# Kernel tuning notes

Hardware: AMD Instinct MI355X
Metric: run time of the kernel (lower is better)

Reference implementation:

```python
import jax, jax.numpy as jnp
import numpy as np
import math

B, T, C = 4, 2048, 1024
N_HEAD = 16


def setup_inputs() -> dict:
    key = jax.random.key(0)
    ks = jax.random.split(key, 5)
    s = 0.02
    return {
        "x": jax.random.normal(ks[0], (B, T, C), jnp.float32),
        "W_attn": jax.random.normal(ks[1], (C, 3 * C), jnp.float32) * s,
        "b_attn": jax.random.normal(ks[2], (3 * C,), jnp.float32) * s,
        "W_proj": jax.random.normal(ks[3], (C, C), jnp.float32) * s,
        "b_proj": jax.random.normal(ks[4], (C,), jnp.float32) * s,
    }


def reference(x, W_attn, b_attn, W_proj, b_proj):
    b, t, c = x.shape
    hd = c // N_HEAD  # head dim
    qkv = x @ W_attn + b_attn                       # [B,T,3C]
    q, k, v = jnp.split(qkv, 3, axis=-1)
    # [B,T,C] -> [B,H,T,hd]
    q = q.reshape(b, t, N_HEAD, hd).transpose(0, 2, 1, 3)
    k = k.reshape(b, t, N_HEAD, hd).transpose(0, 2, 1, 3)
    v = v.reshape(b, t, N_HEAD, hd).transpose(0, 2, 1, 3)
    att = jnp.einsum("bhqd,bhkd->bhqk", q, k) * (1.0 / math.sqrt(hd))
    causal = jnp.tril(jnp.ones((t, t), dtype=bool))
    att = jnp.where(causal, att, -jnp.inf)
    att = jax.nn.softmax(att, axis=-1)              # dropout disabled (eval mode)
    y = jnp.einsum("bhqk,bhkd->bhqd", att, v)       # [B,H,T,hd]
    y = y.transpose(0, 2, 1, 3).reshape(b, t, c)
    out = y @ W_proj + b_proj                       # resid dropout disabled (eval)
    return out
```

## Files before the change

### kernel.cpp

```cpp
#include <hip/hip_runtime.h>

#define B_  4
#define T_  2048
#define C_  1024
#define H_  16
#define D_  64
#define BT_ 8192

typedef __bf16 bf16x8 __attribute__((ext_vector_type(8)));
typedef float  f32x4  __attribute__((ext_vector_type(4)));

#define MFMA(a, b, c) __builtin_amdgcn_mfma_f32_16x16x32_bf16((a), (b), (c), 0, 0, 0)
#define LOG2E 1.4426950408889634f

__device__ __forceinline__ float fexp2(float x) {
#if __has_builtin(__builtin_amdgcn_exp2f)
    return __builtin_amdgcn_exp2f(x);
#else
    return __expf(x * 0.6931471805599453f);
#endif
}

__device__ __forceinline__ unsigned short f2bf(float f) {
    union { float f; unsigned u; } v; v.f = f;
    unsigned r = v.u + 0x7FFFu + ((v.u >> 16) & 1u);
    return (unsigned short)(r >> 16);
}

__device__ __forceinline__ void gll16(const unsigned short* g, unsigned short* l) {
    __builtin_amdgcn_global_load_lds((const __attribute__((address_space(1))) void*)g,
                                     (__attribute__((address_space(3))) void*)l, 16, 0, 0);
}

template <int GPR>
__device__ __forceinline__ void stage16(const unsigned short* grow0, size_t stride_us,
                                        unsigned short* lds, int chunk) {
    const int lane = threadIdx.x & 63;
    const int gidx = chunk * 64 + lane;
    const int row  = gidx / GPR, c = gidx % GPR;
    const int csrc = c ^ (row & (GPR - 1));
    gll16(grow0 + (size_t)row * stride_us + csrc * 8, lds + gidx * 8);
}

__global__ __launch_bounds__(256) void prep_kernel(const float* __restrict__ x,
                                                   unsigned short* __restrict__ xb,
                                                   const float* __restrict__ Wa,
                                                   unsigned short* __restrict__ Wab,
                                                   const float* __restrict__ Wp,
                                                   unsigned short* __restrict__ Wpb) {
    __shared__ float tile[32][33];
    const int bid = blockIdx.x;
    if (bid < 8192) {
        int i = bid * 1024 + threadIdx.x * 4;
        float4 v = *(const float4*)&x[i];
        ushort4 o;
        o.x = f2bf(v.x); o.y = f2bf(v.y); o.z = f2bf(v.z); o.w = f2bf(v.w);
        *(ushort4*)&xb[i] = o;
        return;
    }
    const float* in; unsigned short* out; int N, t;
    if (bid < 11264) { t = bid - 8192;  in = Wa; out = Wab; N = 3072; }
    else             { t = bid - 11264; in = Wp; out = Wpb; N = 1024; }
    const int n0 = (t % (N / 32)) * 32, k0 = (t / (N / 32)) * 32;
    const int tr = threadIdx.x >> 3, tc = (threadIdx.x & 7) * 4;
    float4 v = *(const float4*)&in[(size_t)(k0 + tr) * N + n0 + tc];
    tile[tr][tc + 0] = v.x; tile[tr][tc + 1] = v.y;
    tile[tr][tc + 2] = v.z; tile[tr][tc + 3] = v.w;
    __syncthreads();
    ushort4 o;
    o.x = f2bf(tile[tc + 0][tr]);
    o.y = f2bf(tile[tc + 1][tr]);
    o.z = f2bf(tile[tc + 2][tr]);
    o.w = f2bf(tile[tc + 3][tr]);
    *(ushort4*)&out[(size_t)(n0 + tr) * 1024 + k0 + tc] = o;
}

__global__ __launch_bounds__(256) void transpose_v_kernel(const unsigned short* __restrict__ qkv,
                                                          unsigned short* __restrict__ vT) {
    __shared__ unsigned short tile[64][65];
    const int bh = blockIdx.y;
    const int b = bh >> 4, h = bh & 15;
    const int t0 = blockIdx.x * 64;
    const size_t src = (size_t)b * 2048 * 3072 + 2048 + h * 64;
    const size_t dbase = (size_t)bh * (T_ * D_);
    const int r = threadIdx.x >> 2, c = (threadIdx.x & 3) * 16;
    uint4 a0 = *(const uint4*)&qkv[src + (size_t)(t0 + r) * 3072 + c];
    uint4 a1 = *(const uint4*)&qkv[src + (size_t)(t0 + r) * 3072 + c + 8];
    const unsigned short* ap = (const unsigned short*)&a0;
    #pragma unroll
    for (int i = 0; i < 8; ++i) tile[r][c + i] = ap[i];
    ap = (const unsigned short*)&a1;
    #pragma unroll
    for (int i = 0; i < 8; ++i) tile[r][c + 8 + i] = ap[i];
    __syncthreads();
    unsigned short tmp[16];
    #pragma unroll
    for (int i = 0; i < 16; ++i) tmp[i] = tile[c + i][r];
    *(uint4*)&vT[dbase + (size_t)r * T_ + t0 + c]     = *(uint4*)&tmp[0];
    *(uint4*)&vT[dbase + (size_t)r * T_ + t0 + c + 8] = *(uint4*)&tmp[8];
}

template <int MODE, int VDIRECT>
__global__ __launch_bounds__(256) void gemm_bf16_kernel(
    const unsigned short* __restrict__ A,
    const unsigned short* __restrict__ Bt,
    const float* __restrict__ bias,
    float* __restrict__ outF,
    unsigned short* __restrict__ outB,
    unsigned short* __restrict__ vTout,
    int M, int N, int K)
{
    __shared__ __align__(16) unsigned short smem[(MODE == 0 && VDIRECT) ? 10240 : 8192];
    unsigned short* As = smem;
    unsigned short* Bs = smem + 4096;
    const int tid = threadIdx.x;
    const int wave = tid >> 6, lane = tid & 63;
    const int wr = wave >> 1, wc = wave & 1;
    const int g = lane >> 4, li = lane & 15;
    const int m0 = blockIdx.y * 128, n0 = blockIdx.x * 128;

    f32x4 acc[4][4] = {};

    for (int k0 = 0; k0 < K; k0 += 32) {
        __syncthreads();
        stage16<4>(A  + (size_t)m0 * K + k0, K, As, wave * 2);
        stage16<4>(A  + (size_t)m0 * K + k0, K, As, wave * 2 + 1);
        stage16<4>(Bt + (size_t)n0 * K + k0, K, Bs, wave * 2);
        stage16<4>(Bt + (size_t)n0 * K + k0, K, Bs, wave * 2 + 1);
        __syncthreads();
        bf16x8 af[4], bfr[4];
        #pragma unroll
        for (int mi = 0; mi < 4; ++mi) {
            const int row = wr * 64 + mi * 16 + li;
            af[mi] = *(const bf16x8*)&As[row * 32 + ((g ^ (row & 3)) * 8)];
        }
        #pragma unroll
        for (int ni = 0; ni < 4; ++ni) {
            const int row = wc * 64 + ni * 16 + li;
            bfr[ni] = *(const bf16x8*)&Bs[row * 32 + ((g ^ (row & 3)) * 8)];
        }
        #pragma unroll
        for (int mi = 0; mi < 4; ++mi)
            #pragma unroll
            for (int ni = 0; ni < 4; ++ni)
                acc[mi][ni] = MFMA(af[mi], bfr[ni], acc[mi][ni]);
    }

    float bb[4];
    #pragma unroll
    for (int ni = 0; ni < 4; ++ni) bb[ni] = bias[n0 + wc * 64 + ni * 16 + li];

    if (MODE == 0) {
        __syncthreads();
        if (VDIRECT && n0 >= 2048) {
            const int h = (n0 - 2048 + wc * 64) >> 6;
            const int b = m0 >> 11;
            const int tb = (m0 & 2047) + wr * 64;
            unsigned short* vstg = smem + wave * 2560;
            #pragma unroll
            for (int mp = 0; mp < 2; ++mp) {
                #pragma unroll
                for (int mh = 0; mh < 2; ++mh) {
                    const int mi = mp * 2 + mh;
                    #pragma unroll
                    for (int ni = 0; ni < 4; ++ni)
                        #pragma unroll
                        for (int r = 0; r < 4; ++r)
                            vstg[(ni * 16 + li) * 40 + mh * 16 + g * 4 + r]
                                = f2bf(acc[mi][ni][r] + bb[ni]);
                }
                __builtin_amdgcn_wave_barrier();
                uint4 w0 = *(const uint4*)&vstg[lane * 40];
                uint4 w1 = *(const uint4*)&vstg[lane * 40 + 8];
                uint4 w2 = *(const uint4*)&vstg[lane * 40 + 16];
                uint4 w3 = *(const uint4*)&vstg[lane * 40 + 24];
                unsigned short* dp = vTout
                    + (((size_t)(b * 16 + h) * 64 + lane) * 2048 + tb + mp * 32);
                *(uint4*)dp = w0; *(uint4*)&dp[8] = w1;
                *(uint4*)&dp[16] = w2; *(uint4*)&dp[24] = w3;
                __builtin_amdgcn_wave_barrier();
            }
        } else {
            unsigned short* stg = smem + wave * 1152;
            const float qsc = (n0 < 1024) ? 0.125f * LOG2E : 1.0f;
            const int srow = lane & 15, scp = lane >> 4;
            #pragma unroll
            for (int mi = 0; mi < 4; ++mi) {
                #pragma unroll
                for (int ni = 0; ni < 4; ++ni)
                    #pragma unroll
                    for (int r = 0; r < 4; ++r)
                        stg[(g * 4 + r) * 72 + ni * 16 + li] = f2bf((acc[mi][ni][r] + bb[ni]) * qsc);
                __builtin_amdgcn_wave_barrier();
                uint4 w0 = *(const uint4*)&stg[srow * 72 + scp * 16];
                uint4 w1 = *(const uint4*)&stg[srow * 72 + scp * 16 + 8];
                unsigned short* dst = &outB[(size_t)(m0 + wr * 64 + mi * 16 + srow) * N
                                            + n0 + wc * 64 + scp * 16];
                *(uint4*)dst = w0;
                *(uint4*)&dst[8] = w1;
                __builtin_amdgcn_wave_barrier();
            }
        }
    } else {
        #pragma unroll
        for (int mi = 0; mi < 4; ++mi)
            #pragma unroll
            for (int ni = 0; ni < 4; ++ni) {
                const int col = n0 + wc * 64 + ni * 16 + li;
                #pragma unroll
                for (int r = 0; r < 4; ++r)
                    outF[(size_t)(m0 + wr * 64 + mi * 16 + g * 4 + r) * N + col]
                        = acc[mi][ni][r] + bb[ni];
            }
    }
}

__global__ __launch_bounds__(256, 4) void flash_attn_kernel(
    const unsigned short* __restrict__ qkv,
    const unsigned short* __restrict__ vT,
    unsigned short* __restrict__ y)
{
    __shared__ __align__(16) unsigned short Ks[2][64 * 64];
    __shared__ __align__(16) unsigned short Vt[2][64 * 64];
    __shared__ __align__(16) unsigned short Pq[4][16][40];
    const int tid = threadIdx.x;
    const int wv = tid >> 6, lane = tid & 63;
    const int g = lane >> 4, li = lane & 15;
    const int bid = blockIdx.x;
    const int xcd = bid & 7, i = bid >> 3;
    const int bh = xcd * 8 + (i & 7);
    const int p  = i >> 3;
    const int qtA = p, qtB = 31 - p;
    const int b = bh >> 4, h = bh & 15;
    const size_t qrowbase = (size_t)b * 2048 * 3072 + h * 64;
    const size_t vbase = (size_t)bh * (D_ * T_);
    const unsigned short* kbase = qkv + qrowbase + 1024;

    const int rowA = qtA * 64 + wv * 16 + li;
    const int rowB = qtB * 64 + wv * 16 + li;

    bf16x8 aqA[2], aqB[2];
    #pragma unroll
    for (int kc = 0; kc < 2; ++kc) {
        aqA[kc] = *(const bf16x8*)&qkv[qrowbase + (size_t)rowA * 3072 + kc * 32 + g * 8];
        aqB[kc] = *(const bf16x8*)&qkv[qrowbase + (size_t)rowB * 3072 + kc * 32 + g * 8];
    }

    f32x4 oA[4] = {}, oB[4] = {};
    float lA = 0.f, lB = 0.f;
    const float OFS = 8.0f * LOG2E;
    const int nkb = qtB + 1;

    stage16<8>(kbase, 3072, Ks[0], wv * 2);
    stage16<8>(kbase, 3072, Ks[0], wv * 2 + 1);
    stage16<8>(vT + vbase, T_, Vt[0], wv * 2);
    stage16<8>(vT + vbase, T_, Vt[0], wv * 2 + 1);

    for (int kb = 0; kb < nkb; ++kb) {
        const int cur = kb & 1;
        __syncthreads();
        if (kb + 1 < nkb) {
            const int kn = (kb + 1) << 6;
            const int nxt = cur ^ 1;
            stage16<8>(kbase + (size_t)kn * 3072, 3072, Ks[nxt], wv * 2);
            stage16<8>(kbase + (size_t)kn * 3072, 3072, Ks[nxt], wv * 2 + 1);
            stage16<8>(vT + vbase + kn, T_, Vt[nxt], wv * 2);
            stage16<8>(vT + vbase + kn, T_, Vt[nxt], wv * 2 + 1);
        }
        const int k0 = kb << 6;
        const bool doA = (kb <= qtA);
        const unsigned short* ksb = Ks[cur];
        const unsigned short* vtb = Vt[cur];

        #pragma unroll
        for (int half = 0; half < 2; ++half) {
            f32x4 sA[2], sB[2];
            #pragma unroll
            for (int t2 = 0; t2 < 2; ++t2) {
                const int krow = (half * 2 + t2) * 16 + li;
                bf16x8 ka0 = *(const bf16x8*)&ksb[krow * 64 + ((g       ^ (krow & 7)) * 8)];
                bf16x8 ka1 = *(const bf16x8*)&ksb[krow * 64 + (((4 + g) ^ (krow & 7)) * 8)];
                f32x4 z = {};
                z = MFMA(ka0, aqB[0], z);
                sB[t2] = MFMA(ka1, aqB[1], z);
                if (doA) {
                    f32x4 z2 = {};
                    z2 = MFMA(ka0, aqA[0], z2);
                    sA[t2] = MFMA(ka1, aqA[1], z2);
                }
            }
            bf16x8 bpA, bpB;
            {
                #pragma unroll
                for (int t2 = 0; t2 < 2; ++t2) {
                    const int kkb = k0 + (half * 2 + t2) * 16;
                    const bool diag = (kb == qtB);
                    ushort4 pw;
                    #pragma unroll
                    for (int r = 0; r < 4; ++r) {
                        float sv = sB[t2][r];
                        if (diag && (kkb + g * 4 + r > rowB)) sv = -1e30f;
                        float pp = fexp2(sv - OFS);
                        lB += pp;
                        ((unsigned short*)&pw)[r] = f2bf(pp);
                    }
                    *(ushort4*)&Pq[wv][li][t2 * 16 + g * 4] = pw;
                }
                __builtin_amdgcn_wave_barrier();
                bpB = *(const bf16x8*)&Pq[wv][li][g * 8];
                __builtin_amdgcn_wave_barrier();
            }
            if (doA) {
                #pragma unroll
                for (int t2 = 0; t2 < 2; ++t2) {
                    const int kkb = k0 + (half * 2 + t2) * 16;
                    const bool diag = (kb == qtA);
                    ushort4 pw;
                    #pragma unroll
                    for (int r = 0; r < 4; ++r) {
                        float sv = sA[t2][r];
                        if (diag && (kkb + g * 4 + r > rowA)) sv = -1e30f;
                        float pp = fexp2(sv - OFS);
                        lA += pp;
                        ((unsigned short*)&pw)[r] = f2bf(pp);
                    }
                    *(ushort4*)&Pq[wv][li][t2 * 16 + g * 4] = pw;
                }
                __builtin_amdgcn_wave_barrier();
                bpA = *(const bf16x8*)&Pq[wv][li][g * 8];
                __builtin_amdgcn_wave_barrier();
            }
            #pragma unroll
            for (int ot = 0; ot < 4; ++ot) {
                const int vrow = ot * 16 + li;
                bf16x8 av = *(const bf16x8*)&vtb[vrow * 64 + (((half * 4 + g) ^ (vrow & 7)) * 8)];
                oB[ot] = MFMA(av, bpB, oB[ot]);
                if (doA) oA[ot] = MFMA(av, bpA, oA[ot]);
            }
            __builtin_amdgcn_wave_barrier();
        }
    }

    #pragma unroll
    for (int t = 0; t < 2; ++t) {
        float l = t ? lB : lA;
        const f32x4* o = t ? oB : oA;
        l += __shfl_xor(l, 16, 64);
        l += __shfl_xor(l, 32, 64);
        float inv = 1.f / l;
        const int trow = (t ? rowB : rowA);
        const size_t yrow = ((size_t)(b * 2048 + trow)) * 1024 + h * 64;
        #pragma unroll
        for (int ot = 0; ot < 4; ++ot) {
            ushort4 pw;
            #pragma unroll
            for (int r = 0; r < 4; ++r)
                ((unsigned short*)&pw)[r] = f2bf(o[ot][r] * inv);
            *(ushort4*)&y[yrow + ot * 16 + g * 4] = pw;
        }
    }
}

extern "C" void kernel_launch(void* const* d_in, const int* in_sizes, int n_in,
                              void* d_out, int out_size, void* d_ws, size_t ws_size,
                              hipStream_t stream)
{
    const float* x      = (const float*)d_in[0];
    const float* W_attn = (const float*)d_in[1];
    const float* b_attn = (const float*)d_in[2];
    const float* W_proj = (const float*)d_in[3];
    const float* b_proj = (const float*)d_in[4];
    float* out = (float*)d_out;

    char* ws = (char*)d_ws;
    size_t off = 0;
    auto alloc = [&](size_t bytes) -> void* {
        void* p = ws + off;
        off += (bytes + 255) & ~(size_t)255;
        return p;
    };
    unsigned short* xb   = (unsigned short*)alloc((size_t)BT_ * C_ * 2);
    unsigned short* Wab  = (unsigned short*)alloc((size_t)3 * C_ * C_ * 2);
    unsigned short* Wpb  = (unsigned short*)alloc((size_t)C_ * C_ * 2);
    unsigned short* qkvb = (unsigned short*)alloc((size_t)BT_ * 3 * C_ * 2);
    unsigned short* yb   = (unsigned short*)alloc((size_t)BT_ * C_ * 2);
    const size_t vt_bytes = (size_t)BT_ * C_ * 2;
    const bool vdirect = (ws_size >= off + vt_bytes);
    unsigned short* vTb = vdirect ? (unsigned short*)alloc(vt_bytes)
                                  : xb;

    prep_kernel<<<12288, 256, 0, stream>>>(x, xb, W_attn, Wab, W_proj, Wpb);

    if (vdirect) {
        gemm_bf16_kernel<0, 1><<<dim3(24, 64), 256, 0, stream>>>(
            xb, Wab, b_attn, nullptr, qkvb, vTb, BT_, 3 * C_, C_);
    } else {
        gemm_bf16_kernel<0, 0><<<dim3(24, 64), 256, 0, stream>>>(
            xb, Wab, b_attn, nullptr, qkvb, nullptr, BT_, 3 * C_, C_);
        transpose_v_kernel<<<dim3(T_ / 64, B_ * H_), 256, 0, stream>>>(qkvb, vTb);
    }

    flash_attn_kernel<<<1024, 256, 0, stream>>>(qkvb, vTb, yb);

    gemm_bf16_kernel<1, 0><<<dim3(8, 64), 256, 0, stream>>>(
        yb, Wpb, b_proj, out, nullptr, nullptr, BT_, C_, C_);
}
```

Measured before the change: 264.1 us.

## Add 256x256-tile 8-wave QKV GEMM with half-tile staged double buffering

Replaces the 128x128 QKV projection GEMM with a dedicated 256x256 tile kernel using 512 threads, swizzled LDS layout, and a ping-pong pipeline that issues global-to-LDS loads in half-tile slices interleaved between MFMA phases with explicit vmcnt waits and priority bumps. Larger tiles raise arithmetic intensity and cut global/L2 traffic, and the fine-grained staging aims to overlap loads with MFMA work. It still fuses bias, the Q scale, and the V transpose into the epilogue. It uses 128KB LDS per block and many accumulator registers, which limits occupancy, and the hand-built barrier and waitcnt schedule carries synchronization risk.

```diff
diff --git a/kernel.cpp b/kernel.cpp
--- a/kernel.cpp
+++ b/kernel.cpp
@@ -212,6 +212,207 @@
                     outF[(size_t)(m0 + wr * 64 + mi * 16 + g * 4 + r) * N + col]
                         = acc[mi][ni][r] + bb[ni];
             }
+    }
+}
+
+
+__device__ __forceinline__ void stage_half64(const unsigned short* g0, int ldk,
+                                             unsigned short* l0, int half) {
+    const int wave = threadIdx.x >> 6, lane = threadIdx.x & 63;
+    #pragma unroll
+    for (int s = 0; s < 2; ++s) {
+        const int h = wave * 2 + s;
+        const int rowbase = (h >> 3) * 128 + half * 64 + (h & 7) * 8;
+        const int row = rowbase + (lane >> 3);
+        const int csrc = (lane & 7) ^ (row & 7);
+        gll16(g0 + (size_t)row * ldk + csrc * 8, l0 + rowbase * 64 + lane * 8);
+    }
+}
+
+#define G2_CLOSE   __builtin_amdgcn_s_barrier()
+#define G2_CLOSE6  do { asm volatile("s_waitcnt vmcnt(6)" ::: "memory"); \
+                        __builtin_amdgcn_s_barrier(); } while (0)
+#define G2_CLOSE0  do { asm volatile("s_waitcnt vmcnt(0)" ::: "memory"); \
+                        __builtin_amdgcn_s_barrier(); } while (0)
+
+#define G2_PHASE(ASB, BSB, MP, STAGE_STMT, CLOSE_STMT) do {                      \
+    if ((MP) == 0) {                                                             \
+        _Pragma("unroll") for (int ni_ = 0; ni_ < 4; ++ni_) {                    \
+            bfr[ni_][0] = *(const bf16x8*)&(BSB)[boff[ni_][0]];                  \
+            bfr[ni_][1] = *(const bf16x8*)&(BSB)[boff[ni_][1]];                  \
+        }                                                                        \
+    }                                                                            \
+    bf16x8 af00 = *(const bf16x8*)&(ASB)[aoff[2 * (MP)][0]];                     \
+    bf16x8 af01 = *(const bf16x8*)&(ASB)[aoff[2 * (MP)][1]];                     \
+    bf16x8 af10 = *(const bf16x8*)&(ASB)[aoff[2 * (MP) + 1][0]];                 \
+    bf16x8 af11 = *(const bf16x8*)&(ASB)[aoff[2 * (MP) + 1][1]];                 \
+    STAGE_STMT;                                                                  \
+    __builtin_amdgcn_sched_barrier(0);     \
+    __builtin_amdgcn_s_barrier();                                                \
+    asm volatile("s_waitcnt lgkmcnt(0)" ::: "memory");                           \
+    __builtin_amdgcn_sched_barrier(0);                                           \
+    __builtin_amdgcn_s_setprio(1);                                               \
+    _Pragma("unroll") for (int ni_ = 0; ni_ < 4; ++ni_) {                        \
+        acc[2 * (MP)][ni_]     = MFMA(af00, bfr[ni_][0], acc[2 * (MP)][ni_]);    \
+        acc[2 * (MP)][ni_]     = MFMA(af01, bfr[ni_][1], acc[2 * (MP)][ni_]);    \
+        acc[2 * (MP) + 1][ni_] = MFMA(af10, bfr[ni_][0], acc[2 * (MP) + 1][ni_]);\
+        acc[2 * (MP) + 1][ni_] = MFMA(af11, bfr[ni_][1], acc[2 * (MP) + 1][ni_]);\
+    }                                                                            \
+    __builtin_amdgcn_s_setprio(0);                                               \
+    CLOSE_STMT;                                                                  \
+  } while (0)
+
+#define G2_KTILE(ASB, BSB, S1, S2, S3, S4, C4) do {                              \
+    bf16x8 bfr[4][2];                                                            \
+    G2_PHASE(ASB, BSB, 0, S1, G2_CLOSE);                                         \
+    G2_PHASE(ASB, BSB, 1, S2, G2_CLOSE);                                         \
+    G2_PHASE(ASB, BSB, 2, S3, G2_CLOSE);                                         \
+    G2_PHASE(ASB, BSB, 3, S4, C4);                                               \
+  } while (0)
+
+__global__ __launch_bounds__(512, 2) void qkv_gemm256_kernel(
+    const unsigned short* __restrict__ A,
+    const unsigned short* __restrict__ Bt,
+    const float* __restrict__ bias,
+    unsigned short* __restrict__ outB,
+    unsigned short* __restrict__ vTout)
+{
+    constexpr int Kc = 1024, Nc = 3072;
+    constexpr int NI = (Kc / 64) / 2;
+    __shared__ __align__(16) unsigned short smem[65536];
+
+    const int tid = threadIdx.x;
+    const int wave = tid >> 6, lane = tid & 63;
+    const int wr = wave >> 2, wc = wave & 3;
+    const int g = lane >> 4, li = lane & 15;
+
+    int bidx, bidy;
+    {
+        const int gx = gridDim.x, gy = gridDim.y;
+        int b = blockIdx.y * gx + blockIdx.x;
+        if ((gy & 7) == 0) {
+            const int gy8 = gy >> 3;
+            const int k = b >> 3;
+            bidy = (b & 7) * gy8 + k / gx;
+            bidx = k - (k / gx) * gx;
+        } else { bidy = blockIdx.y; bidx = blockIdx.x; }
+    }
+    const int m0 = bidy * 256, n0 = bidx * 256;
+
+    unsigned short* As0 = smem;
+    unsigned short* Bs0 = smem + 16384;
+    unsigned short* As1 = smem + 32768;
+    unsigned short* Bs1 = smem + 49152;
+
+    const unsigned short* Ag = A  + (size_t)m0 * Kc;
+    const unsigned short* Bg = Bt + (size_t)n0 * Kc;
+
+    int aoff[8][2], boff[4][2];
+    #pragma unroll
+    for (int mi = 0; mi < 8; ++mi) {
+        const int R = wr * 128 + mi * 16 + li;
+        #pragma unroll
+        for (int kk = 0; kk < 2; ++kk)
+            aoff[mi][kk] = R * 64 + (((kk * 4 + g) ^ (R & 7)) * 8);
+    }
+    #pragma unroll
+    for (int ni = 0; ni < 4; ++ni) {
+        const int R = wc * 64 + ni * 16 + li;
+        #pragma unroll
+        for (int kk = 0; kk < 2; ++kk)
+            boff[ni][kk] = R * 64 + (((kk * 4 + g) ^ (R & 7)) * 8);
+    }
+
+    f32x4 acc[8][4] = {};
+
+    stage_half64(Bg,      Kc, Bs0, 0);
+    stage_half64(Bg,      Kc, Bs0, 1);
+    stage_half64(Ag,      Kc, As0, 0);
+    stage_half64(Ag,      Kc, As0, 1);
+    stage_half64(Bg + 64, Kc, Bs1, 0);
+    stage_half64(Bg + 64, Kc, Bs1, 1);
+    stage_half64(Ag + 64, Kc, As1, 0);
+    asm volatile("s_waitcnt vmcnt(6)" ::: "memory");
+    __builtin_amdgcn_s_barrier();
+
+    #pragma unroll 1
+    for (int i = 0; i < NI - 1; ++i) {
+        const int kA  = (2 * i + 1) * 64;
+        const int kB0 = (2 * i + 2) * 64;
+        const int kB1 = (2 * i + 3) * 64;
+        G2_KTILE(As0, Bs0,
+                 stage_half64(Ag + kA,  Kc, As1, 1),
+                 stage_half64(Bg + kB0, Kc, Bs0, 0),
+                 stage_half64(Bg + kB0, Kc, Bs0, 1),
+                 stage_half64(Ag + kB0, Kc, As0, 0),
+                 G2_CLOSE6);
+        G2_KTILE(As1, Bs1,
+                 stage_half64(Ag + kB0, Kc, As0, 1),
+                 stage_half64(Bg + kB1, Kc, Bs1, 0),
+                 stage_half64(Bg + kB1, Kc, Bs1, 1),
+                 stage_half64(Ag + kB1, Kc, As1, 0),
+                 G2_CLOSE6);
+    }
+    G2_KTILE(As0, Bs0,
+             stage_half64(Ag + (Kc - 64), Kc, As1, 1),
+             (void)0, (void)0, (void)0,
+             G2_CLOSE0);
+    G2_KTILE(As1, Bs1, (void)0, (void)0, (void)0, (void)0, G2_CLOSE);
+
+    __syncthreads();
+
+    float bb[4];
+    #pragma unroll
+    for (int ni = 0; ni < 4; ++ni) bb[ni] = bias[n0 + wc * 64 + ni * 16 + li];
+
+    if (n0 >= 2048) {
+        const int h  = ((n0 - 2048) >> 6) + wc;
+        const int b  = m0 >> 11;
+        const int tb = (m0 & 2047) + wr * 128;
+        unsigned short* vstg = smem + wave * 2560;
+        #pragma unroll
+        for (int mp = 0; mp < 4; ++mp) {
+            #pragma unroll
+            for (int mh = 0; mh < 2; ++mh) {
+                const int mi = mp * 2 + mh;
+                #pragma unroll
+                for (int ni = 0; ni < 4; ++ni)
+                    #pragma unroll
+                    for (int r = 0; r < 4; ++r)
+                        vstg[(ni * 16 + li) * 40 + mh * 16 + g * 4 + r]
+                            = f2bf(acc[mi][ni][r] + bb[ni]);
+            }
+            __builtin_amdgcn_wave_barrier();
+            uint4 w0 = *(const uint4*)&vstg[lane * 40];
+            uint4 w1 = *(const uint4*)&vstg[lane * 40 + 8];
+            uint4 w2 = *(const uint4*)&vstg[lane * 40 + 16];
+            uint4 w3 = *(const uint4*)&vstg[lane * 40 + 24];
+            unsigned short* dp = vTout
+                + (((size_t)(b * 16 + h) * 64 + lane) * 2048 + tb + mp * 32);
+            *(uint4*)dp = w0; *(uint4*)&dp[8] = w1;
+            *(uint4*)&dp[16] = w2; *(uint4*)&dp[24] = w3;
+            __builtin_amdgcn_wave_barrier();
+        }
+    } else {
+        unsigned short* stg = smem + wave * 1152;
+        const float qsc = (n0 < 1024) ? 0.125f * LOG2E : 1.0f;
+        const int srow = lane & 15, scp = lane >> 4;
+        #pragma unroll
+        for (int mi = 0; mi < 8; ++mi) {
+            #pragma unroll
+            for (int ni = 0; ni < 4; ++ni)
+                #pragma unroll
+                for (int r = 0; r < 4; ++r)
+                    stg[(g * 4 + r) * 72 + ni * 16 + li] = f2bf((acc[mi][ni][r] + bb[ni]) * qsc);
+            __builtin_amdgcn_wave_barrier();
+            uint4 w0 = *(const uint4*)&stg[srow * 72 + scp * 16];
+            uint4 w1 = *(const uint4*)&stg[srow * 72 + scp * 16 + 8];
+            unsigned short* dst = &outB[(size_t)(m0 + wr * 128 + mi * 16 + srow) * Nc
+                                        + n0 + wc * 64 + scp * 16];
+            *(uint4*)dst = w0;
+            *(uint4*)&dst[8] = w1;
+            __builtin_amdgcn_wave_barrier();
+        }
     }
 }
 
@@ -392,8 +593,8 @@
     prep_kernel<<<12288, 256, 0, stream>>>(x, xb, W_attn, Wab, W_proj, Wpb);
 
     if (vdirect) {
-        gemm_bf16_kernel<0, 1><<<dim3(24, 64), 256, 0, stream>>>(
-            xb, Wab, b_attn, nullptr, qkvb, vTb, BT_, 3 * C_, C_);
+        qkv_gemm256_kernel<<<dim3(12, 32), 512, 0, stream>>>(
+            xb, Wab, b_attn, qkvb, vTb);
     } else {
         gemm_bf16_kernel<0, 0><<<dim3(24, 64), 256, 0, stream>>>(
             xb, Wab, b_attn, nullptr, qkvb, nullptr, BT_, 3 * C_, C_);
```

New measurement: 257.4 us. 1.03x faster.
